# Optimization experiments

Measured on AMD Instinct MI355X. Metric: run time of the kernel, lower is better.

The kernel has to match this reference:

```python
import jax, jax.numpy as jnp
import numpy as np

K = 3
HALF = K // 2  # original code uses python2-style k/2 integer division
NUM_CLASSES = 201
IDENTITY = jnp.array([1.0, 0.0, 0.0, 0.0, 1.0, 0.0], dtype=jnp.float32)

def conv2d(x, w, b, pad):
    y = jax.lax.conv_general_dilated(x, w, (1, 1), [(pad, pad), (pad, pad)],
                                     dimension_numbers=('NCHW', 'OIHW', 'NCHW'))
    return y if b is None else y + b[None, :, None, None]

def affine_grid(theta, k):
    # F.affine_grid, align_corners=True (old-torch default matching the /(H-1) normalization)
    base = jnp.linspace(-1.0, 1.0, k, dtype=theta.dtype)
    xb = base[None, None, :]  # varies along width
    yb = base[None, :, None]  # varies along height
    gx = theta[:, 0, 0, None, None] * xb + theta[:, 0, 1, None, None] * yb + theta[:, 0, 2, None, None]
    gy = theta[:, 1, 0, None, None] * xb + theta[:, 1, 1, None, None] * yb + theta[:, 1, 2, None, None]
    return jnp.stack([gx, gy], axis=-1)  # [N, k, k, 2]

def make_aux(grid, B, S, H, W):
    # per-location absolute sampling coords, renormalized to [-1,1] over the full map
    off = HALF + jnp.arange(S, dtype=grid.dtype)
    gx = (grid[..., 0] * HALF).reshape(B, S, S, K, K) + off[None, :, None, None, None]
    gy = (grid[..., 1] * HALF).reshape(B, S, S, K, K) + off[None, None, :, None, None]
    auxx = gx.reshape(-1, K, K) / (H - 1) * 2.0 - 1.0
    auxy = gy.reshape(-1, K, K) / (W - 1) * 2.0 - 1.0
    return auxx, auxy

def grid_sample(x, grid, bidx):
    # bilinear, align_corners=True, zero padding; avoids materializing tile(x,0,S*S)
    B, C, H, W = x.shape
    gx = (grid[..., 0] + 1.0) * 0.5 * (W - 1)
    gy = (grid[..., 1] + 1.0) * 0.5 * (H - 1)
    x0 = jnp.floor(gx); y0 = jnp.floor(gy)
    wx1 = gx - x0; wy1 = gy - y0
    def gather(yi, xi):
        valid = (yi >= 0) & (yi <= H - 1) & (xi >= 0) & (xi <= W - 1)
        yc = jnp.clip(yi, 0, H - 1).astype(jnp.int32)
        xc = jnp.clip(xi, 0, W - 1).astype(jnp.int32)
        v = x[bidx[:, None, None], :, yc, xc]  # [N, k, k, C]
        return v * valid[..., None]
    out = (gather(y0, x0) * ((1 - wy1) * (1 - wx1))[..., None]
         + gather(y0, x0 + 1) * ((1 - wy1) * wx1)[..., None]
         + gather(y0 + 1, x0) * (wy1 * (1 - wx1))[..., None]
         + gather(y0 + 1, x0 + 1) * (wy1 * wx1)[..., None])
    return jnp.transpose(out, (0, 3, 1, 2))  # [N, C, k, k]

def compute_scores(x, p, check):
    B, C, H, W = x.shape
    h = jax.nn.relu(conv2d(x, p['stn0_w'], p['stn0_b'], HALF))
    out = conv2d(h, p['stn1_w'], None, 0) * (1.0 - check) + IDENTITY[None, :, None, None]
    S = out.shape[2]  # square maps assumed (required by original view logic)
    theta = jnp.transpose(out, (0, 3, 2, 1)).reshape(-1, 2, 3)  # flatten order (b, w, h)
    grid = affine_grid(theta, K)
    auxx, auxy = make_aux(grid, B, S, H, W)
    auxgrid = jnp.stack([auxx, auxy], axis=3)
    bidx = jnp.repeat(jnp.arange(B), S * S)
    xs = grid_sample(x, auxgrid, bidx)  # [B*S*S, C, K, K]
    feat = xs.reshape(xs.shape[0], -1) @ p['conv_w'].T + p['conv_b']
    output = jnp.transpose(feat.reshape(B, S, S, -1), (0, 3, 2, 1))
    output = jnp.einsum('bfhw,of->bohw', jax.nn.relu(output), p['last_w']) + p['last_b'][None, :, None, None]
    return output, theta, auxx, auxy, S

def box_from_aux(auxx, auxy, dl, conf, image_dim):
    tx = ((auxx + 1.0) * 0.5).reshape(auxx.shape[0], -1)[dl]
    ty = ((auxy + 1.0) * 0.5).reshape(auxy.shape[0], -1)[dl]
    lo, hi = 0.0, image_dim - 1
    return jnp.stack([jnp.clip(tx.min(1) * image_dim, lo, hi),
                      jnp.clip(ty.min(1) * image_dim, lo, hi),
                      jnp.clip(tx.max(1) * image_dim, lo, hi),
                      jnp.clip(ty.max(1) * image_dim, lo, hi),
                      conf], axis=1)

def max_boxes(l, pred, S, auxx, auxy, image_dim):
    B = l.shape[0]
    scores = l[jnp.arange(B), pred]          # [B, S*S]
    dl0 = jnp.argmax(scores, axis=1)
    conf = jnp.max(scores, axis=1)
    dl = (dl0 % S) * S + dl0 // S + jnp.arange(B) * (S * S)  # swap (h,w)->(w,h) flat index
    return box_from_aux(auxx, auxy, dl, conf, image_dim), dl, conf

def nt_aux(B, S, H, W):
    grid0 = affine_grid(IDENTITY.reshape(1, 2, 3), K)
    grid = jnp.broadcast_to(grid0, (B * S * S, K, K, 2))
    return make_aux(grid, B, S, H, W)

def _forward(x0, x1, p, check, image_dim):
    B = x0.shape[0]
    s5, th5, ax5, ay5, S5 = compute_scores(x0, p, check)
    s4, th4, ax4, ay4, S4 = compute_scores(x1, p, check)
    theta_diff = jnp.concatenate([IDENTITY.reshape(1, 2, 3) - th5,
                                  IDENTITY.reshape(1, 2, 3) - th4], axis=0)
    sc5 = s5.reshape(B, NUM_CLASSES, -1)
    sc4 = s4.reshape(B, NUM_CLASSES, -1)
    score = jnp.concatenate([sc5, sc4], axis=2)
    joint = jax.nn.softmax(score.reshape(B, -1), axis=1).reshape(B, NUM_CLASSES, -1)
    likelihood = joint.sum(2)
    L5 = sc5.shape[2]
    l5 = joint[:, :, :L5]
    l4 = joint[:, :, L5:]
    pred = jnp.argmax(likelihood, axis=1)
    sg = jax.lax.stop_gradient  # torch.no_grad block
    box5, dl5, conf5 = max_boxes(sg(l5), pred, S5, sg(ax5), sg(ay5), image_dim)
    ntx5, nty5 = nt_aux(B, S5, x0.shape[2], x0.shape[3])
    boxNT5 = box_from_aux(ntx5, nty5, dl5, conf5, image_dim)
    box4, dl4, conf4 = max_boxes(sg(l4), pred, S4, sg(ax4), sg(ay4), image_dim)
    ntx4, nty4 = nt_aux(B, S4, x1.shape[2], x1.shape[3])
    boxNT4 = box_from_aux(ntx4, nty4, dl4, conf4, image_dim)
    boxes = jnp.stack([box5, box4], axis=1)       # [B, 2, 5]
    boxes_NT = jnp.stack([boxNT5, boxNT4], axis=1)
    mi = jnp.argmax(boxes[:, :, 4], axis=1)
    boxes = boxes[jnp.arange(B), mi]
    boxes_NT = boxes_NT[jnp.arange(B), mi]
    max_l5 = jnp.max(l5[jnp.arange(B), pred], axis=1)
    max_l4 = jnp.max(l4[jnp.arange(B), pred], axis=1)
    reg_score = jnp.sum(jnp.maximum(0.0, max_l4 - max_l5))
    return likelihood, boxes, boxes_NT, theta_diff, reg_score

def setup_inputs() -> dict:
    key = jax.random.key(0)
    ks = jax.random.split(key, 10)
    B, C, F = 32, 256, 1024
    x0 = jax.random.normal(ks[0], (B, C, 10, 10), jnp.float32)
    x1 = jax.random.normal(ks[1], (B, C, 20, 20), jnp.float32)
    stn0_w = jax.random.normal(ks[2], (C, C, 3, 3), jnp.float32) * 0.02
    stn0_b = jax.random.normal(ks[3], (C,), jnp.float32) * 0.01
    stn1_w = jax.random.normal(ks[4], (6, C, 3, 3), jnp.float32) * 0.01
    conv_w = jax.random.normal(ks[5], (F, C * K * K), jnp.float32) * 0.02
    conv_b = jax.random.normal(ks[6], (F,), jnp.float32) * 0.01
    last_w = jax.random.normal(ks[7], (NUM_CLASSES, F), jnp.float32) * 0.03
    last_b = jax.random.normal(ks[8], (NUM_CLASSES,), jnp.float32) * 0.01
    return {'x0': x0, 'x1': x1, 'stn0_w': stn0_w, 'stn0_b': stn0_b, 'stn1_w': stn1_w,
            'conv_w': conv_w, 'conv_b': conv_b, 'last_w': last_w, 'last_b': last_b,
            'check': 0, 'image_dim': 320}

def reference(x0, x1, stn0_w, stn0_b, stn1_w, conv_w, conv_b, last_w, last_b, check, image_dim):
    p = {'stn0_w': stn0_w, 'stn0_b': stn0_b, 'stn1_w': stn1_w,
         'conv_w': conv_w, 'conv_b': conv_b, 'last_w': last_w, 'last_b': last_b}
    return _forward(x0, x1, p, float(check), image_dim)
```

## Files before the change

### kernel.cpp

```cpp
#include <hip/hip_runtime.h>
#include <cmath>

#define TPB 256

constexpr int Bb = 32, Cc = 256, Ff = 1024, Oo = 201;
constexpr int H0 = 10, S0 = 8,  N0 = Bb * S0 * S0;
constexpr int H1 = 20, S1 = 18, N1 = Bb * S1 * S1;
constexpr int NT_ALL = N0 + N1;
constexpr int KC = Cc * 9;
constexpr int KP = Cc * 16;
constexpr int L5 = S0 * S0, L4 = S1 * S1, LT = L5 + L4;
constexpr int CHMAX = 4224;
constexpr int M1 = Bb * H0 * H0;
constexpr int MCONV = M1 + Bb * H1 * H1;

constexpr size_t SZ_CW  = (size_t)Ff * KC;
constexpr size_t SZ_W0P = (size_t)Cc * KP;
constexpr size_t SZ_LWP = (size_t)256 * Ff;

constexpr size_t B_CWH = 0;
constexpr size_t B_CWL = B_CWH + SZ_CW * 2;
constexpr size_t B_GXY = B_CWL + SZ_CW * 2;
constexpr size_t B_LWH = B_GXY + (size_t)NT_ALL * 18 * 4;
constexpr size_t B_LWL = B_LWH + SZ_LWP * 2;
constexpr size_t B_SC  = B_LWL + SZ_LWP * 2;
constexpr size_t B_XSH = B_SC + (size_t)Bb * Oo * LT * 4;
constexpr size_t B_XSL = B_XSH + (size_t)CHMAX * KC * 2;
constexpr size_t B_FCH = B_XSL + (size_t)CHMAX * KC * 2;
constexpr size_t B_FCL = B_FCH + (size_t)CHMAX * Ff * 2;
constexpr size_t B_MX  = B_FCL + (size_t)CHMAX * Ff * 2;
constexpr size_t B_SM  = B_MX + 128;
constexpr size_t B_RP  = B_SM + 128;
constexpr size_t B_END = B_RP + 128;
constexpr size_t B_W0H = B_XSH;
constexpr size_t B_W0L = B_XSH + SZ_W0P * 2;
constexpr size_t B_H0  = B_XSL;
constexpr size_t B_H1  = B_XSL + (size_t)Bb * Cc * H0 * H0 * 4;
constexpr size_t B_C2  = B_FCH;

constexpr size_t O_LIK = 0;
constexpr size_t O_BOX = O_LIK + Bb * Oo;
constexpr size_t O_NT  = O_BOX + Bb * 5;
constexpr size_t O_TD  = O_NT + Bb * 5;
constexpr size_t O_REG = O_TD + (size_t)NT_ALL * 6;

typedef __attribute__((ext_vector_type(8))) short bf16x8;
typedef __attribute__((ext_vector_type(4))) float f32x4;

__device__ __forceinline__ void tsplit(float v, short& h, short& l) {
    unsigned u = __builtin_bit_cast(unsigned, v);
    h = (short)(u >> 16);
    float hf = __builtin_bit_cast(float, u & 0xffff0000u);
    float r = v - hf;
    l = (short)(__builtin_bit_cast(unsigned, r) >> 16);
}
__device__ __forceinline__ float clampf(float x, float lo, float hi) {
    return fminf(fmaxf(x, lo), hi);
}
__device__ __forceinline__ void gload16(const void* g, void* l) {
    __builtin_amdgcn_global_load_lds(
        (const __attribute__((address_space(1))) void*)g,
        (__attribute__((address_space(3))) void*)l, 16, 0, 0);
}
__device__ __forceinline__ size_t aidx(int row, int k, int KD) {
    return ((size_t)(row >> 7) * (KD >> 5) + (k >> 5)) * 4096
         + (size_t)(((row & 127) >> 4) * 512 + ((k >> 3) & 3) * 128 + (row & 15) * 8 + (k & 7));
}

__global__ __launch_bounds__(TPB)
void splitp_k(const float* __restrict__ src, short* __restrict__ hi,
              short* __restrict__ lo, int nrows)
{
    int idx = blockIdx.x * TPB + threadIdx.x;
    if (idx >= nrows * 288) return;
    int row = idx / 288, r = idx - row * 288;
    int t = r >> 5, cg = r & 31;
    const float* sp = src + (size_t)row * KC + (size_t)cg * 8 * 9 + t;
    bf16x8 hv, lv;
    #pragma unroll
    for (int e = 0; e < 8; e++) {
        short h, l; tsplit(sp[e * 9], h, l);
        hv[e] = h; lv[e] = l;
    }
    size_t dst = aidx(row, t * 256 + cg * 8, KC);
    *(bf16x8*)&hi[dst] = hv;
    *(bf16x8*)&lo[dst] = lv;
}

__global__ __launch_bounds__(TPB)
void splitp16_k(const float* __restrict__ src, short* __restrict__ hi,
                short* __restrict__ lo, int nrows)
{
    int idx = blockIdx.x * TPB + threadIdx.x;
    if (idx >= nrows * KP) return;
    int row = idx >> 12, kq = idx & (KP - 1);
    int c = kq >> 4, t = kq & 15;
    float v = (t < 9) ? src[(size_t)row * KC + c * 9 + t] : 0.f;
    short h, l; tsplit(v, h, l);
    hi[idx] = h; lo[idx] = l;
}

__global__ __launch_bounds__(TPB)
void splitlw_k(const float* __restrict__ src, short* __restrict__ hi,
               short* __restrict__ lo)
{
    int idx = blockIdx.x * TPB + threadIdx.x;
    if (idx >= (int)SZ_LWP) return;
    int row = idx >> 10, k = idx & 1023;
    float v = (row < Oo) ? src[idx] : 0.f;
    short h, l; tsplit(v, h, l);
    size_t dst = aidx(row, k, Ff);
    hi[dst] = h; lo[dst] = l;
}

__global__ __launch_bounds__(TPB)
void mat_k(const float* __restrict__ x0, const float* __restrict__ x1,
           const float* __restrict__ gxy, short* __restrict__ xsH,
           short* __restrict__ xsL, int base, int rows)
{
    int idx = blockIdx.x * TPB + threadIdx.x;
    if (idx >= rows * 288) return;
    int mloc = idx / 288, r = idx - mloc * 288;
    int j = r >> 5, cg = r & 31;
    int m = base + mloc;
    const float* xp; int H, loc, SS;
    if (m < N0) { xp = x0; H = H0; loc = m; SS = 64; }
    else        { xp = x1; H = H1; loc = m - N0; SS = 324; }
    int b = loc / SS;
    float gx = gxy[(size_t)m * 18 + j];
    float gy = gxy[(size_t)m * 18 + 9 + j];
    float xf = floorf(gx), yf = floorf(gy);
    float wx = gx - xf, wy = gy - yf;
    int ix = (int)xf, iy = (int)yf;
    int cx0 = min(max(ix, 0), H - 1), cy0 = min(max(iy, 0), H - 1);
    bool vx0 = (ix >= 0 && ix < H), vx1 = (ix >= -1 && ix < H - 1);
    bool vy0 = (iy >= 0 && iy < H), vy1 = (iy >= -1 && iy < H - 1);
    float wxL = vx0 ? (1.f - wx) : (vx1 ? wx : 0.f);
    float wxR = (vx0 && vx1) ? wx : 0.f;
    float wyT = vy0 ? (1.f - wy) : (vy1 ? wy : 0.f);
    float wyB = (vy0 && vy1) ? wy : 0.f;
    float wTL = wyT * wxL, wTR = wyT * wxR, wBL = wyB * wxL, wBR = wyB * wxR;
    int o   = cy0 * H + cx0;
    int oTR = (wTR != 0.f) ? o + 1     : o;
    int oBL = (wBL != 0.f) ? o + H     : o;
    int oBR = (wBR != 0.f) ? o + H + 1 : o;
    const float* cp = xp + ((size_t)b * Cc + cg * 8) * (H * H);
    bf16x8 hv, lv;
    #pragma unroll
    for (int e = 0; e < 8; e++) {
        float v = cp[o] * wTL + cp[oTR] * wTR + cp[oBL] * wBL + cp[oBR] * wBR;
        short h, l; tsplit(v, h, l); hv[e] = h; lv[e] = l;
        cp += H * H;
    }
    size_t dst = aidx(mloc, j * 256 + cg * 8, KC);
    *(bf16x8*)&xsH[dst] = hv;
    *(bf16x8*)&xsL[dst] = lv;
}

template<int MODE, int KD>
__global__ __launch_bounds__(TPB, 4)
void mgemm(const float* __restrict__ x0s, const float* __restrict__ x1s,
           const short* __restrict__ Bh, const short* __restrict__ Bl,
           const float* __restrict__ bias,
           float* __restrict__ outF, float* __restrict__ outF2)
{
    __shared__ short As[2][4][128][8];
    __shared__ short Bs[2][4][32][8];
    __shared__ float slab[1600];

    const int tid = threadIdx.x;
    const int lane = tid & 63;
    const int wid = tid >> 6;
    const int wm = (wid >> 1) * 64, wn = (wid & 1) * 16;
    const int ml = tid & 127, kg0 = tid >> 7;
    const int bm = blockIdx.y * 128, bn = blockIdx.x * 32;

    f32x4 acc[4];
    #pragma unroll
    for (int i = 0; i < 4; i++) acc[i] = (f32x4){0.f, 0.f, 0.f, 0.f};

    const float* xsrc = nullptr;
    int Hh = 0, PLSZr = 0, UPPr = 0, bat0 = 0, batidx = 0, nu = 0;
    float wvt[9]; int offt[9];
    {
        int lbase;
        if (bm < M1) { xsrc = x0s; Hh = H0; lbase = bm; }
        else         { xsrc = x1s; Hh = H1; lbase = bm - M1; }
        PLSZr = Hh * Hh; UPPr = PLSZr >> 2;
        int mGl = lbase + ml;
        int bA = mGl / PLSZr; int rem = mGl - bA * PLSZr;
        int yA = rem / Hh, xA = rem - (rem / Hh) * Hh;
        bat0 = lbase / PLSZr;
        int nb = (lbase + 127) / PLSZr - bat0 + 1;
        batidx = bA - bat0;
        nu = nb * 2 * UPPr;
        #pragma unroll
        for (int t = 0; t < 9; t++) {
            int ky = t / 3 - 1, kx = t - (t / 3) * 3 - 1;
            int yy = yA + ky, xx = xA + kx;
            bool ok = (yy >= 0 && yy < Hh && xx >= 0 && xx < Hh);
            offt[t] = ok ? (yy * Hh + xx) : 0;
            wvt[t] = ok ? 1.f : 0.f;
        }
    }

    float4 rv0 = {}, rv1 = {}, rv2 = {};
    float4 pv0 = {}, pv1 = {}, pv2 = {};
    auto issue_loads = [&](int kb, float4& a0, float4& a1, float4& a2) {
        const int c0 = kb >> 4;
        #pragma unroll
        for (int q = 0; q < 3; q++) {
            int i = tid + q * TPB;
            if (i < nu) {
                int pl = i / UPPr, u = i - pl * UPPr;
                int bi = pl >> 1, cc = pl & 1;
                float4 v = *(const float4*)(xsrc +
                    ((size_t)(bat0 + bi) * Cc + c0 + cc) * PLSZr + u * 4);
                if (q == 0) a0 = v; else if (q == 1) a1 = v; else a2 = v;
            }
        }
    };
    auto write_slab = [&](const float4& a0, const float4& a1, const float4& a2) {
        #pragma unroll
        for (int q = 0; q < 3; q++) {
            int i = tid + q * TPB;
            if (i < nu)
                *(float4*)&slab[i * 4] = (q == 0) ? a0 : (q == 1) ? a1 : a2;
        }
    };

    issue_loads(0, rv0, rv1, rv2);

    for (int kb = 0; kb < KD; kb += 32) {
        write_slab(rv0, rv1, rv2);
        if (kb + 32 < KD) issue_loads(kb + 32, pv0, pv1, pv2);
        __syncthreads();
        #pragma unroll
        for (int s8 = 0; s8 < 2; s8++) {
            int s = wid + s8 * 4;
            int hilo = s & 1, kg = s >> 1;
            if (lane < 32) {
                const short* g = (hilo ? Bl : Bh) + (size_t)(bn + lane) * KD + kb + kg * 8;
                gload16(g, &Bs[hilo][kg][0][0]);
            }
        }
        const float* sp = &slab[(batidx * 2 + kg0) * PLSZr];
        bf16x8 hv, lv;
        #pragma unroll
        for (int e = 0; e < 8; e++) {
            float v = sp[offt[e]] * wvt[e];
            short h, l; tsplit(v, h, l); hv[e] = h; lv[e] = l;
        }
        *(bf16x8*)&As[0][kg0 * 2][ml][0] = hv;
        *(bf16x8*)&As[1][kg0 * 2][ml][0] = lv;
        bf16x8 hv2 = {}, lv2 = {};
        { float v = sp[offt[8]] * wvt[8];
          short h, l; tsplit(v, h, l); hv2[0] = h; lv2[0] = l; }
        *(bf16x8*)&As[0][kg0 * 2 + 1][ml][0] = hv2;
        *(bf16x8*)&As[1][kg0 * 2 + 1][ml][0] = lv2;
        __syncthreads();
        {
            const int kq = lane >> 4, r = lane & 15;
            bf16x8 ah[4], al[4];
            #pragma unroll
            for (int i = 0; i < 4; i++) {
                ah[i] = *(const bf16x8*)&As[0][kq][wm + i * 16 + r][0];
                al[i] = *(const bf16x8*)&As[1][kq][wm + i * 16 + r][0];
            }
            bf16x8 bh = *(const bf16x8*)&Bs[0][kq][wn + r][0];
            bf16x8 bl = *(const bf16x8*)&Bs[1][kq][wn + r][0];
            #pragma unroll
            for (int i = 0; i < 4; i++) {
                acc[i] = __builtin_amdgcn_mfma_f32_16x16x32_bf16(ah[i], bh, acc[i], 0, 0, 0);
                acc[i] = __builtin_amdgcn_mfma_f32_16x16x32_bf16(al[i], bh, acc[i], 0, 0, 0);
                acc[i] = __builtin_amdgcn_mfma_f32_16x16x32_bf16(ah[i], bl, acc[i], 0, 0, 0);
            }
        }
        rv0 = pv0; rv1 = pv1; rv2 = pv2;
    }

    const int kq = lane >> 4, rr = lane & 15;
    #pragma unroll
    for (int i = 0; i < 4; i++) {
        #pragma unroll
        for (int r = 0; r < 4; r++) {
            const int gm = bm + wm + i * 16 + kq * 4 + r;
            const int gn = bn + wn + rr;
            float v = acc[i][r];
            float* hp; int Hq, lr;
            if (gm < M1) { hp = outF; Hq = H0; lr = gm; }
            else         { hp = outF2; Hq = H1; lr = gm - M1; }
            int PL = Hq * Hq;
            int bq = lr / PL; int rem = lr - bq * PL;
            int yq = rem / Hq; int xq = rem - yq * Hq;
            hp[((size_t)bq * Cc + gn) * PL + yq * Hq + xq] = fmaxf(v + bias[gn], 0.f);
        }
    }
}

template<int MODE, int KD>
__global__ __launch_bounds__(TPB, 3)
void mgemm4(const short* __restrict__ AsH_, const short* __restrict__ AsL_,
            const short* __restrict__ Bh, const short* __restrict__ Bl,
            const float* __restrict__ bias,
            float* __restrict__ outF, short* __restrict__ outH,
            short* __restrict__ outL, int base)
{
    constexpr int NSTEP = KD / 32;
    const int tid = threadIdx.x;
    const int lane = tid & 63;
    const int wid = tid >> 6;
    const int wm = (wid >> 1) * 64, wn = (wid & 1) * 32;
    const int bm = blockIdx.y * 128, bn = blockIdx.x * 64;

    const size_t ablk0 = (size_t)(bm >> 7) * NSTEP * 4096;
    const size_t bblk0 = (size_t)(bn >> 7) * NSTEP * 4096;
    const int ai = wm >> 4;
    const int bi = ((bn & 64) + wn) >> 4;
    const int lo8 = lane * 8;

    f32x4 acc[4][2];
    #pragma unroll
    for (int i = 0; i < 4; i++)
        #pragma unroll
        for (int j = 0; j < 2; j++)
            acc[i][j] = (f32x4){0.f, 0.f, 0.f, 0.f};

    bf16x8 Ah[2][4], Al[2][4], Bhf[2][2], Blf[2][2];

    auto LOAD = [&](int s, int t) {
        const size_t ab = ablk0 + (size_t)t * 4096;
        const size_t bb = bblk0 + (size_t)t * 4096;
        #pragma unroll
        for (int i = 0; i < 4; i++) {
            Ah[s][i] = *(const bf16x8*)(AsH_ + ab + (ai + i) * 512 + lo8);
            Al[s][i] = *(const bf16x8*)(AsL_ + ab + (ai + i) * 512 + lo8);
        }
        #pragma unroll
        for (int j = 0; j < 2; j++) {
            Bhf[s][j] = *(const bf16x8*)(Bh + bb + (bi + j) * 512 + lo8);
            Blf[s][j] = *(const bf16x8*)(Bl + bb + (bi + j) * 512 + lo8);
        }
    };
    auto MM = [&](int s) {
        #pragma unroll
        for (int i = 0; i < 4; i++)
            #pragma unroll
            for (int j = 0; j < 2; j++) {
                acc[i][j] = __builtin_amdgcn_mfma_f32_16x16x32_bf16(Ah[s][i], Bhf[s][j], acc[i][j], 0, 0, 0);
                acc[i][j] = __builtin_amdgcn_mfma_f32_16x16x32_bf16(Al[s][i], Bhf[s][j], acc[i][j], 0, 0, 0);
                acc[i][j] = __builtin_amdgcn_mfma_f32_16x16x32_bf16(Ah[s][i], Blf[s][j], acc[i][j], 0, 0, 0);
            }
    };

    LOAD(0, 0);
    for (int t = 0; t < NSTEP; t += 2) {
        LOAD(1, t + 1);
        MM(0);
        if (t + 2 < NSTEP) LOAD(0, t + 2);
        MM(1);
    }

    const int kq = lane >> 4, rr = lane & 15;
    #pragma unroll
    for (int i = 0; i < 4; i++) {
        #pragma unroll
        for (int r = 0; r < 4; r++) {
            const int gm = bm + wm + i * 16 + kq * 4 + r;
            #pragma unroll
            for (int j = 0; j < 2; j++) {
                const int gn = bn + wn + j * 16 + rr;
                float v = acc[i][j][r];
                if constexpr (MODE == 4) {
                    float q = fmaxf(v + bias[gn], 0.f);
                    short h, l; tsplit(q, h, l);
                    size_t d = aidx(gm, gn, Ff);
                    outH[d] = h;
                    outL[d] = l;
                } else {
                    if (gn < Oo) {
                        int g = base + gm;
                        int bq, pos;
                        if (g < N0) {
                            int lo = g & 63; bq = g >> 6;
                            pos = (lo & 7) * 8 + (lo >> 3);
                        } else {
                            int gg = g - N0; bq = gg / 324; int lo = gg - bq * 324;
                            int xq = lo / 18, yq = lo - xq * 18;
                            pos = L5 + yq * 18 + xq;
                        }
                        outF[((size_t)bq * Oo + gn) * LT + pos] = v + bias[gn];
                    }
                }
            }
        }
    }
}

__global__ __launch_bounds__(TPB)
void conv2_k(const float* __restrict__ h0, const float* __restrict__ h1,
             const float* __restrict__ w1, float* __restrict__ c2)
{
    __shared__ float wl[6][KC];
    __shared__ float part[8][32][6];
    const int tid = threadIdx.x;
    for (int i = tid; i < 6 * KC; i += TPB) wl[i / KC][i - (i / KC) * KC] = w1[i];
    __syncthreads();
    const int row = blockIdx.x * 32 + (tid & 31);
    const int cig = tid >> 5;
    const float* hsrc; int H, S, loc;
    if (row < N0) { hsrc = h0; H = H0; S = S0; loc = row; }
    else          { hsrc = h1; H = H1; S = S1; loc = row - N0; }
    int SS = S * S;
    int b = loc / SS; int rem = loc - b * SS;
    int xq = rem / S; int yq = rem - xq * S;
    float acc[6] = {};
    for (int ci = cig * 32; ci < cig * 32 + 32; ci++) {
        const float* hp = hsrc + ((size_t)(b * Cc + ci) * H + yq) * H + xq;
        #pragma unroll
        for (int ky = 0; ky < 3; ky++)
            #pragma unroll
            for (int kx = 0; kx < 3; kx++) {
                float a = hp[ky * H + kx];
                int kk = ci * 9 + ky * 3 + kx;
                #pragma unroll
                for (int n = 0; n < 6; n++) acc[n] = fmaf(a, wl[n][kk], acc[n]);
            }
    }
    #pragma unroll
    for (int n = 0; n < 6; n++) part[cig][tid & 31][n] = acc[n];
    __syncthreads();
    if (cig == 0) {
        #pragma unroll
        for (int n = 0; n < 6; n++) {
            float s = 0.f;
            for (int g = 0; g < 8; g++) s += part[g][tid & 31][n];
            c2[(size_t)row * 6 + n] = s;
        }
    }
}

__global__ __launch_bounds__(TPB)
void theta_aux_k(const float* __restrict__ c2, const int* __restrict__ checkp,
                 float* __restrict__ td, float* __restrict__ gxy)
{
    int n = blockIdx.x * TPB + threadIdx.x;
    if (n >= NT_ALL) return;
    float omc = 1.0f - (float)checkp[0];
    const float I[6] = {1.f, 0.f, 0.f, 0.f, 1.f, 0.f};
    float th[6];
    #pragma unroll
    for (int i = 0; i < 6; i++) {
        float v = c2[(size_t)n * 6 + i] * omc + I[i];
        th[i] = v;
        td[(size_t)n * 6 + i] = I[i] - v;
    }
    int S, loc;
    if (n < N0) { S = S0; loc = n; } else { S = S1; loc = n - N0; }
    int SS = S * S;
    int rem = loc % SS;
    int xx = rem / S, yy = rem % S;
    #pragma unroll
    for (int ky = 0; ky < 3; ky++)
        #pragma unroll
        for (int kx = 0; kx < 3; kx++) {
            float bx = (float)(kx - 1), by = (float)(ky - 1);
            gxy[(size_t)n * 18 + ky * 3 + kx]     = th[0] * bx + th[1] * by + th[2] + 1.0f + (float)xx;
            gxy[(size_t)n * 18 + 9 + ky * 3 + kx] = th[3] * bx + th[4] * by + th[5] + 1.0f + (float)yy;
        }
}

__global__ __launch_bounds__(TPB)
void statslik_k(const float* __restrict__ sc, float* __restrict__ mx,
                float* __restrict__ sm, float* __restrict__ lik)
{
    int b = blockIdx.x, tid = threadIdx.x;
    const float* p = sc + (size_t)b * Oo * LT;
    constexpr int PER = Oo * LT;
    __shared__ float red[TPB];
    float m = -3.4e38f;
    for (int i = tid; i < PER; i += TPB) m = fmaxf(m, p[i]);
    red[tid] = m;
    for (int off = 128; off; off >>= 1) { __syncthreads(); if (tid < off) red[tid] = fmaxf(red[tid], red[tid + off]); }
    __syncthreads();
    m = red[0];
    __syncthreads();
    float so = 0.f;
    if (tid < Oo) {
        const float* q = p + (size_t)tid * LT;
        for (int i = 0; i < LT; i++) so += expf(q[i] - m);
    }
    red[tid] = so;
    for (int off = 128; off; off >>= 1) { __syncthreads(); if (tid < off) red[tid] += red[tid + off]; }
    __syncthreads();
    float smt = red[0];
    if (tid < Oo) lik[b * Oo + tid] = so / smt;
    if (tid == 0) { mx[b] = m; sm[b] = smt; }
}

__global__ __launch_bounds__(TPB)
void box_k(const float* __restrict__ sc, const float* __restrict__ lik,
           const float* __restrict__ mx, const float* __restrict__ sm,
           const float* __restrict__ gxy, const int* __restrict__ imdp,
           float* __restrict__ boxes, float* __restrict__ boxesNT,
           float* __restrict__ regpart)
{
    int b = blockIdx.x, tid = threadIdx.x;
    __shared__ float sv[TPB];
    __shared__ int si[TPB];

    float v = (tid < Oo) ? lik[b * Oo + tid] : -3.4e38f;
    sv[tid] = v; si[tid] = tid;
    for (int off = 128; off; off >>= 1) {
        __syncthreads();
        if (tid < off) {
            float v2 = sv[tid + off]; int i2 = si[tid + off];
            if (v2 > sv[tid] || (v2 == sv[tid] && i2 < si[tid])) { sv[tid] = v2; si[tid] = i2; }
        }
    }
    __syncthreads();
    int pred = si[0];
    __syncthreads();

    const float* p = sc + ((size_t)b * Oo + pred) * LT;
    float b5 = -3.4e38f; int i5 = 1 << 30;
    float b4 = -3.4e38f; int i4 = 1 << 30;
    for (int pos = tid; pos < LT; pos += TPB) {
        float s = p[pos];
        if (pos < L5) { if (s > b5) { b5 = s; i5 = pos; } }
        else { int q = pos - L5; if (s > b4) { b4 = s; i4 = q; } }
    }
    sv[tid] = b5; si[tid] = i5;
    for (int off = 128; off; off >>= 1) {
        __syncthreads();
        if (tid < off) {
            float v2 = sv[tid + off]; int i2 = si[tid + off];
            if (v2 > sv[tid] || (v2 == sv[tid] && i2 < si[tid])) { sv[tid] = v2; si[tid] = i2; }
        }
    }
    __syncthreads();
    float m5 = sv[0]; int d5 = si[0];
    __syncthreads();
    sv[tid] = b4; si[tid] = i4;
    for (int off = 128; off; off >>= 1) {
        __syncthreads();
        if (tid < off) {
            float v2 = sv[tid + off]; int i2 = si[tid + off];
            if (v2 > sv[tid] || (v2 == sv[tid] && i2 < si[tid])) { sv[tid] = v2; si[tid] = i2; }
        }
    }
    __syncthreads();
    float m4 = sv[0]; int d4 = si[0];

    if (tid == 0) {
        float m = mx[b], s = sm[b];
        float conf5 = expf(m5 - m) / s;
        float conf4 = expf(m4 - m) / s;
        float imd = (float)imdp[0];
        float lo = 0.f, hi = imd - 1.f;

        int xx5 = d5 % S0, yy5 = d5 / S0;
        int n5 = b * (S0 * S0) + xx5 * S0 + yy5;
        const float* g = gxy + (size_t)n5 * 18;
        float txm = 1e30f, txM = -1e30f, tym = 1e30f, tyM = -1e30f;
        for (int j = 0; j < 9; j++) {
            float tx = g[j] / 9.f, ty = g[9 + j] / 9.f;
            txm = fminf(txm, tx); txM = fmaxf(txM, tx);
            tym = fminf(tym, ty); tyM = fmaxf(tyM, ty);
        }
        float box5[5] = { clampf(txm * imd, lo, hi), clampf(tym * imd, lo, hi),
                          clampf(txM * imd, lo, hi), clampf(tyM * imd, lo, hi), conf5 };
        float nt5[5]  = { clampf((float)xx5 / 9.f * imd, lo, hi), clampf((float)yy5 / 9.f * imd, lo, hi),
                          clampf((float)(xx5 + 2) / 9.f * imd, lo, hi), clampf((float)(yy5 + 2) / 9.f * imd, lo, hi), conf5 };

        int xx4 = d4 % S1, yy4 = d4 / S1;
        int n4 = N0 + b * (S1 * S1) + xx4 * S1 + yy4;
        const float* g4 = gxy + (size_t)n4 * 18;
        float txm4 = 1e30f, txM4 = -1e30f, tym4 = 1e30f, tyM4 = -1e30f;
        for (int j = 0; j < 9; j++) {
            float tx = g4[j] / 19.f, ty = g4[9 + j] / 19.f;
            txm4 = fminf(txm4, tx); txM4 = fmaxf(txM4, tx);
            tym4 = fminf(tym4, ty); tyM4 = fmaxf(tyM4, ty);
        }
        float box4[5] = { clampf(txm4 * imd, lo, hi), clampf(tym4 * imd, lo, hi),
                          clampf(txM4 * imd, lo, hi), clampf(tyM4 * imd, lo, hi), conf4 };
        float nt4[5]  = { clampf((float)xx4 / 19.f * imd, lo, hi), clampf((float)yy4 / 19.f * imd, lo, hi),
                          clampf((float)(xx4 + 2) / 19.f * imd, lo, hi), clampf((float)(yy4 + 2) / 19.f * imd, lo, hi), conf4 };

        int mi = (conf4 > conf5) ? 1 : 0;
        for (int i = 0; i < 5; i++) {
            boxes[b * 5 + i]   = mi ? box4[i] : box5[i];
            boxesNT[b * 5 + i] = mi ? nt4[i] : nt5[i];
        }
        regpart[b] = fmaxf(conf4 - conf5, 0.f);
    }
}

__global__ void reg_k(const float* __restrict__ regpart, float* __restrict__ outreg)
{
    if (threadIdx.x == 0) {
        float s = 0.f;
        for (int b = 0; b < Bb; b++) s += regpart[b];
        outreg[0] = s;
    }
}

__global__ void sentinel_k(float* out, int n)
{
    int i = blockIdx.x * 256 + threadIdx.x;
    if (i < n) out[i] = 12345.0f;
}

extern "C" void kernel_launch(void* const* d_in, const int* in_sizes, int n_in,
                              void* d_out, int out_size, void* d_ws, size_t ws_size,
                              hipStream_t stream)
{
    const float* x0 = (const float*)d_in[0];
    const float* x1 = (const float*)d_in[1];
    const float* w0 = (const float*)d_in[2];
    const float* b0 = (const float*)d_in[3];
    const float* w1 = (const float*)d_in[4];
    const float* cw = (const float*)d_in[5];
    const float* cb = (const float*)d_in[6];
    const float* lw = (const float*)d_in[7];
    const float* lb = (const float*)d_in[8];
    const int* checkp = (const int*)d_in[9];
    const int* imdp   = (const int*)d_in[10];

    if (ws_size < B_END) {
        sentinel_k<<<dim3((out_size + 255) / 256), dim3(256), 0, stream>>>((float*)d_out, out_size);
        return;
    }

    char* wsb = (char*)d_ws;
    short* cwh = (short*)(wsb + B_CWH);
    short* cwl = (short*)(wsb + B_CWL);
    float* gxy = (float*)(wsb + B_GXY);
    short* lwh = (short*)(wsb + B_LWH);
    short* lwl = (short*)(wsb + B_LWL);
    float* sc  = (float*)(wsb + B_SC);
    short* xsH = (short*)(wsb + B_XSH);
    short* xsL = (short*)(wsb + B_XSL);
    short* fcH = (short*)(wsb + B_FCH);
    short* fcL = (short*)(wsb + B_FCL);
    float* mx  = (float*)(wsb + B_MX);
    float* sm  = (float*)(wsb + B_SM);
    float* rp  = (float*)(wsb + B_RP);
    short* w0h = (short*)(wsb + B_W0H);
    short* w0l = (short*)(wsb + B_W0L);
    float* h0  = (float*)(wsb + B_H0);
    float* h1  = (float*)(wsb + B_H1);
    float* c2  = (float*)(wsb + B_C2);

    float* out   = (float*)d_out;
    float* o_lik = out + O_LIK;
    float* o_box = out + O_BOX;
    float* o_nt  = out + O_NT;
    float* o_td  = out + O_TD;
    float* o_reg = out + O_REG;

    dim3 blk(TPB);

    splitp_k  <<<dim3((Ff * 288 + TPB - 1) / TPB), blk, 0, stream>>>(cw, cwh, cwl, Ff);
    splitp16_k<<<dim3((int)((SZ_W0P + TPB - 1) / TPB)), blk, 0, stream>>>(w0, w0h, w0l, Cc);
    splitlw_k <<<dim3((int)((SZ_LWP + TPB - 1) / TPB)), blk, 0, stream>>>(lw, lwh, lwl);

    mgemm<0, KP><<<dim3(8, MCONV / 128), blk, 0, stream>>>(
        x0, x1, w0h, w0l, b0, h0, h1);

    conv2_k<<<dim3(NT_ALL / 32), blk, 0, stream>>>(h0, h1, w1, c2);

    theta_aux_k<<<dim3((NT_ALL + TPB - 1) / TPB), blk, 0, stream>>>(c2, checkp, o_td, gxy);

    const int bases[3] = {0, 4096, 8192};
    const int sizes[3] = {4096, 4096, 4224};
    for (int c = 0; c < 3; c++) {
        int basei = bases[c], rows = sizes[c];
        int mt = rows / 128;
        mat_k<<<dim3((rows * 288 + TPB - 1) / TPB), blk, 0, stream>>>(
            x0, x1, gxy, xsH, xsL, basei, rows);
        mgemm4<4, KC><<<dim3(16, mt), blk, 0, stream>>>(
            xsH, xsL, cwh, cwl, cb, nullptr, fcH, fcL, 0);
        mgemm4<5, Ff><<<dim3(4, mt), blk, 0, stream>>>(
            fcH, fcL, lwh, lwl, lb, sc, nullptr, nullptr, basei);
    }

    statslik_k<<<dim3(Bb), blk, 0, stream>>>(sc, mx, sm, o_lik);
    box_k<<<dim3(Bb), blk, 0, stream>>>(sc, o_lik, mx, sm, gxy, imdp, o_box, o_nt, rp);
    reg_k<<<dim3(1), dim3(64), 0, stream>>>(rp, o_reg);
}
```

Baseline: 920.9 us.

## Widen first-conv GEMM tile to 128x64 with 512-thread blocks

The implicit-GEMM kernel for the first 3x3 conv now uses 512 threads and covers 64 output channels per block instead of 32, halving the grid's N dimension. Each input slab is loaded and expanded into the A tile once per 64 channels rather than once per 32, which cuts redundant gather, split and global-load work. The im2col work is split so half the threads build the 8 full taps and the other half build the ninth-tap chunk. Larger blocks use more registers and LDS per block and give fewer blocks in flight.

```diff
diff --git a/kernel.cpp b/kernel.cpp
--- a/kernel.cpp
+++ b/kernel.cpp
@@ -2,6 +2,7 @@
 #include <cmath>
 
 #define TPB 256
+#define TPB2 512
 
 constexpr int Bb = 32, Cc = 256, Ff = 1024, Oo = 201;
 constexpr int H0 = 10, S0 = 8,  N0 = Bb * S0 * S0;
@@ -157,23 +158,25 @@
     *(bf16x8*)&xsL[dst] = lv;
 }
 
-template<int MODE, int KD>
-__global__ __launch_bounds__(TPB, 4)
+template<int KD>
+__global__ __launch_bounds__(TPB2, 4)
 void mgemm(const float* __restrict__ x0s, const float* __restrict__ x1s,
            const short* __restrict__ Bh, const short* __restrict__ Bl,
            const float* __restrict__ bias,
            float* __restrict__ outF, float* __restrict__ outF2)
 {
     __shared__ short As[2][4][128][8];
-    __shared__ short Bs[2][4][32][8];
+    __shared__ short Bs[2][4][64][8];
     __shared__ float slab[1600];
 
     const int tid = threadIdx.x;
     const int lane = tid & 63;
     const int wid = tid >> 6;
-    const int wm = (wid >> 1) * 64, wn = (wid & 1) * 16;
-    const int ml = tid & 127, kg0 = tid >> 7;
-    const int bm = blockIdx.y * 128, bn = blockIdx.x * 32;
+    const int wm = (wid >> 2) * 64, wn = (wid & 3) * 16;
+    const int ml = tid & 127;
+    const int cc = (tid >> 7) & 1;
+    const int half = tid >> 8;
+    const int bm = blockIdx.y * 128, bn = blockIdx.x * 64;
 
     f32x4 acc[4];
     #pragma unroll
@@ -204,60 +207,61 @@
         }
     }
 
-    float4 rv0 = {}, rv1 = {}, rv2 = {};
-    float4 pv0 = {}, pv1 = {}, pv2 = {};
-    auto issue_loads = [&](int kb, float4& a0, float4& a1, float4& a2) {
+    float4 rv0 = {}, rv1 = {};
+    float4 pv0 = {}, pv1 = {};
+    auto issue_loads = [&](int kb, float4& a0, float4& a1) {
         const int c0 = kb >> 4;
         #pragma unroll
-        for (int q = 0; q < 3; q++) {
-            int i = tid + q * TPB;
+        for (int q = 0; q < 2; q++) {
+            int i = tid + q * TPB2;
             if (i < nu) {
                 int pl = i / UPPr, u = i - pl * UPPr;
-                int bi = pl >> 1, cc = pl & 1;
+                int bi = pl >> 1, ccq = pl & 1;
                 float4 v = *(const float4*)(xsrc +
-                    ((size_t)(bat0 + bi) * Cc + c0 + cc) * PLSZr + u * 4);
-                if (q == 0) a0 = v; else if (q == 1) a1 = v; else a2 = v;
+                    ((size_t)(bat0 + bi) * Cc + c0 + ccq) * PLSZr + u * 4);
+                if (q == 0) a0 = v; else a1 = v;
             }
         }
     };
-    auto write_slab = [&](const float4& a0, const float4& a1, const float4& a2) {
-        #pragma unroll
-        for (int q = 0; q < 3; q++) {
-            int i = tid + q * TPB;
+    auto write_slab = [&](const float4& a0, const float4& a1) {
+        #pragma unroll
+        for (int q = 0; q < 2; q++) {
+            int i = tid + q * TPB2;
             if (i < nu)
-                *(float4*)&slab[i * 4] = (q == 0) ? a0 : (q == 1) ? a1 : a2;
+                *(float4*)&slab[i * 4] = (q == 0) ? a0 : a1;
         }
     };
 
-    issue_loads(0, rv0, rv1, rv2);
+    issue_loads(0, rv0, rv1);
 
     for (int kb = 0; kb < KD; kb += 32) {
-        write_slab(rv0, rv1, rv2);
-        if (kb + 32 < KD) issue_loads(kb + 32, pv0, pv1, pv2);
+        write_slab(rv0, rv1);
+        if (kb + 32 < KD) issue_loads(kb + 32, pv0, pv1);
         __syncthreads();
-        #pragma unroll
-        for (int s8 = 0; s8 < 2; s8++) {
-            int s = wid + s8 * 4;
-            int hilo = s & 1, kg = s >> 1;
-            if (lane < 32) {
-                const short* g = (hilo ? Bl : Bh) + (size_t)(bn + lane) * KD + kb + kg * 8;
-                gload16(g, &Bs[hilo][kg][0][0]);
+        {
+            int hilo = wid & 1, kg = wid >> 1;
+            const short* g = (hilo ? Bl : Bh) + (size_t)(bn + lane) * KD + kb + kg * 8;
+            gload16(g, &Bs[hilo][kg][0][0]);
+        }
+        {
+            const float* sp = &slab[(batidx * 2 + cc) * PLSZr];
+            if (half == 0) {
+                bf16x8 hv, lv;
+                #pragma unroll
+                for (int e = 0; e < 8; e++) {
+                    float v = sp[offt[e]] * wvt[e];
+                    short h, l; tsplit(v, h, l); hv[e] = h; lv[e] = l;
+                }
+                *(bf16x8*)&As[0][cc * 2][ml][0] = hv;
+                *(bf16x8*)&As[1][cc * 2][ml][0] = lv;
+            } else {
+                bf16x8 hv2 = {}, lv2 = {};
+                float v = sp[offt[8]] * wvt[8];
+                short h, l; tsplit(v, h, l); hv2[0] = h; lv2[0] = l;
+                *(bf16x8*)&As[0][cc * 2 + 1][ml][0] = hv2;
+                *(bf16x8*)&As[1][cc * 2 + 1][ml][0] = lv2;
             }
         }
-        const float* sp = &slab[(batidx * 2 + kg0) * PLSZr];
-        bf16x8 hv, lv;
-        #pragma unroll
-        for (int e = 0; e < 8; e++) {
-            float v = sp[offt[e]] * wvt[e];
-            short h, l; tsplit(v, h, l); hv[e] = h; lv[e] = l;
-        }
-        *(bf16x8*)&As[0][kg0 * 2][ml][0] = hv;
-        *(bf16x8*)&As[1][kg0 * 2][ml][0] = lv;
-        bf16x8 hv2 = {}, lv2 = {};
-        { float v = sp[offt[8]] * wvt[8];
-          short h, l; tsplit(v, h, l); hv2[0] = h; lv2[0] = l; }
-        *(bf16x8*)&As[0][kg0 * 2 + 1][ml][0] = hv2;
-        *(bf16x8*)&As[1][kg0 * 2 + 1][ml][0] = lv2;
         __syncthreads();
         {
             const int kq = lane >> 4, r = lane & 15;
@@ -276,7 +280,7 @@
                 acc[i] = __builtin_amdgcn_mfma_f32_16x16x32_bf16(ah[i], bl, acc[i], 0, 0, 0);
             }
         }
-        rv0 = pv0; rv1 = pv1; rv2 = pv2;
+        rv0 = pv0; rv1 = pv1;
     }
 
     const int kq = lane >> 4, rr = lane & 15;
@@ -665,7 +669,7 @@
     splitp16_k<<<dim3((int)((SZ_W0P + TPB - 1) / TPB)), blk, 0, stream>>>(w0, w0h, w0l, Cc);
     splitlw_k <<<dim3((int)((SZ_LWP + TPB - 1) / TPB)), blk, 0, stream>>>(lw, lwh, lwl);
 
-    mgemm<0, KP><<<dim3(8, MCONV / 128), blk, 0, stream>>>(
+    mgemm<KP><<<dim3(4, MCONV / 128), dim3(TPB2), 0, stream>>>(
         x0, x1, w0h, w0l, b0, h0, h1);
 
     conv2_k<<<dim3(NT_ALL / 32), blk, 0, stream>>>(h0, h1, w1, c2);
```

After: 864.3 us. 1.07x faster.
